# Performance work log

Measured on AMD Instinct MI355X. Metric: run time of the kernel, lower is better.

Reference implementation:

```python
import jax, jax.numpy as jnp
import numpy as np

N = 65536   # query points
M = 65536   # support points
H = 32      # neighbors per query
IN = 64     # input feature dim
OUT = 64    # out_dim // 2
K = 15      # kernel points
EXTENT = 0.1 * 1.2 / 2.5  # radius * kp_extent / conv_radius = 0.048
BN_EPS = 1e-5


def setup_inputs() -> dict:
    key = jax.random.key(0)
    ks = jax.random.split(key, 8)
    x = jax.random.normal(ks[0], (M, IN), dtype=jnp.float32)
    q_pts = jax.random.uniform(ks[1], (N, 3), dtype=jnp.float32) * 0.1
    s_pts = jax.random.uniform(ks[2], (M, 3), dtype=jnp.float32) * 0.1
    neighb_inds = jax.random.randint(ks[3], (N, H), 0, M, dtype=jnp.int32)
    kernel_points = jax.random.normal(ks[4], (K, 3), dtype=jnp.float32) * (0.5 * EXTENT)
    weights = jax.random.normal(ks[5], (K, IN, OUT), dtype=jnp.float32) * 0.05
    gamma = jnp.ones((OUT,), dtype=jnp.float32)
    beta = jnp.zeros((OUT,), dtype=jnp.float32)
    return {"x": x, "q_pts": q_pts, "s_pts": s_pts, "neighb_inds": neighb_inds,
            "kernel_points": kernel_points, "weights": weights,
            "gamma": gamma, "beta": beta}


def reference(x, q_pts, s_pts, neighb_inds, kernel_points, weights, gamma, beta):
    # --- KPConv (rigid, linear influence, sum aggregation) ---
    # Shadow point/feature for out-of-range neighbor indices (KPConv convention).
    s_pad = jnp.concatenate([s_pts, jnp.full((1, 3), 1e6, s_pts.dtype)], axis=0)
    x_pad = jnp.concatenate([x, jnp.zeros((1, x.shape[1]), x.dtype)], axis=0)

    # Relative neighbor coordinates: [N, H, 3]
    neighbors = s_pad[neighb_inds] - q_pts[:, None, :]
    # Squared distance to each kernel point: [N, H, K]
    diffs = neighbors[:, :, None, :] - kernel_points[None, None, :, :]
    sq_dist = jnp.sum(diffs * diffs, axis=-1)
    # Linear kernel-point influence, clipped at 0: [N, H, K]
    all_weights = jnp.maximum(1.0 - jnp.sqrt(sq_dist) / EXTENT, 0.0)

    # Gather neighbor features: [N, H, IN]
    neighb_x = x_pad[neighb_inds]
    # Influence-weighted aggregation per kernel point: [N, K, IN]
    weighted = jnp.einsum('nhk,nhi->nki', all_weights, neighb_x)
    # Apply per-kernel-point weight matrices and sum over kernel points: [N, OUT]
    out = jnp.einsum('nki,kio->no', weighted, weights)

    # --- BatchNorm (training-mode statistics over points) ---
    mean = jnp.mean(out, axis=0)
    var = jnp.var(out, axis=0)
    out = (out - mean) / jnp.sqrt(var + BN_EPS) * gamma + beta

    # --- LeakyReLU(0.1) ---
    return jnp.where(out >= 0, out, 0.1 * out)
```

## Files before the change

kernel.cpp:

```cpp
#include <hip/hip_runtime.h>
#include <math.h>

#define NQ   65536
#define H    32
#define IN   64
#define OUTC 64
#define K    15
#define QB   16
#define S_XN 68
#define S_WT 36
#define AK   72
#define AROW 1076
#define INV_EXT (1.0f / 0.048f)

#define OFF_PSUM  131072
#define OFF_SCSH  (OFF_PSUM + 2097152)
#define OFF_XBF   (OFF_SCSH + 1024)
#define NEED_BF16 (OFF_XBF + (size_t)NQ * IN * 2)

typedef __attribute__((ext_vector_type(8))) short short8;
typedef __attribute__((ext_vector_type(4))) short short4v;
typedef __attribute__((ext_vector_type(4))) float float4v;

static __device__ __forceinline__ unsigned short f2bf(float f) {
    return (unsigned short)((__float_as_uint(f) + 0x8000u) >> 16);
}
static __device__ __forceinline__ unsigned pk2(float a, float b) {
    return (__float_as_uint(a) + 0x8000u) >> 16 |
           ((__float_as_uint(b) + 0x8000u) & 0xFFFF0000u);
}

__global__ __launch_bounds__(256) void prep_all(
    const float* __restrict__ W, const float* __restrict__ x,
    short* __restrict__ Bfrag, unsigned short* __restrict__ xbf, int do_x)
{
    const int b = blockIdx.x;
    if (b < 4096) {
        if (do_x) {
            const int t = b * 256 + threadIdx.x;
            const float4 v = ((const float4*)x)[t];
            uint2 p; p.x = pk2(v.x, v.y); p.y = pk2(v.z, v.w);
            ((uint2*)xbf)[t] = p;
        }
    } else {
        const int t2 = (b - 4096) * 256 + threadIdx.x;
        const int o  = t2 & 63;
        const int i  = (t2 >> 6) & 63;
        const int kq = t2 >> 12;
        const int t  = kq * 2 + (i >> 5);
        const int lane = ((i >> 3) & 3) * 16 + (o & 15);
        const int v  = o >> 4;
        const int j  = i & 7;
        Bfrag[((v * 30 + t) * 64 + lane) * 8 + j] = (short)f2bf(W[t2]);
    }
}

template<bool BFX>
__global__ __launch_bounds__(256, 4) void kpconv_mfma(
    const float* __restrict__ x, const unsigned short* __restrict__ xbf,
    const float* __restrict__ qp, const float* __restrict__ sp,
    const int* __restrict__ inds, const float* __restrict__ kp,
    const short* __restrict__ Bfrag, float* __restrict__ out_raw,
    float* __restrict__ psum)
{
    __shared__ __align__(16) short lds[17920];
    short* xn  = lds;
    short* wT  = lds + 8704;
    short* Awt = lds;

    const int tid  = threadIdx.x;
    const int lane = tid & 63;
    const int wv   = tid >> 6;
    const int quad = lane >> 4;
    const int ml   = lane & 15;
    const int q0   = blockIdx.x * QB;

    for (int rep = 0; rep < 2; ++rep) {
        const int pair = tid + rep * 256;
        const int q = pair >> 5, h = pair & 31;
        const int n = q0 + q;
        const int id = inds[n * H + h];
        const float dx = sp[id * 3 + 0] - qp[n * 3 + 0];
        const float dy = sp[id * 3 + 1] - qp[n * 3 + 1];
        const float dz = sp[id * 3 + 2] - qp[n * 3 + 2];
#pragma unroll
        for (int k = 0; k < K; ++k) {
            const float ex = dx - kp[k * 3 + 0];
            const float ey = dy - kp[k * 3 + 1];
            const float ez = dz - kp[k * 3 + 2];
            const float sq = ex * ex + ey * ey + ez * ez;
            float wval = 1.0f - __builtin_amdgcn_sqrtf(sq) * INV_EXT;
            wval = wval > 0.0f ? wval : 0.0f;
            wT[(q * 16 + k) * S_WT + h] = (short)f2bf(wval);
        }
        wT[(q * 16 + K) * S_WT + h] = 0;
    }
    __syncthreads();

    float4v frag[QB];
#pragma unroll
    for (int qg = 0; qg < QB; ++qg) frag[qg] = (float4v){0.f, 0.f, 0.f, 0.f};

    for (int b = 0; b < 4; ++b) {
        const int qg_s = 4 * b + wv;
        const int ibase = (q0 + qg_s) * H;
#pragma unroll
        for (int j = 0; j < 8; ++j) {
            const int h = j * 4 + quad;
            const int id = inds[ibase + h];
            if (BFX) {
                const short4v xv = *(const short4v*)((const short*)xbf + id * IN + ml * 4);
                *(short4v*)&xn[(wv * H + h) * S_XN + ml * 4] = xv;
            } else {
                const float4 xv = *(const float4*)(x + id * IN + ml * 4);
                short4v p;
                p[0] = (short)f2bf(xv.x); p[1] = (short)f2bf(xv.y);
                p[2] = (short)f2bf(xv.z); p[3] = (short)f2bf(xv.w);
                *(short4v*)&xn[(wv * H + h) * S_XN + ml * 4] = p;
            }
        }
        __syncthreads();
#pragma unroll
        for (int ql = 0; ql < 4; ++ql) {
            const int qg = 4 * b + ql;
            const int arow = (qg * 16 + ml) * S_WT + quad * 8;
            const short4v alo = *(const short4v*)&wT[arow];
            const short4v ahi = *(const short4v*)&wT[arow + 4];
            short8 a;
#pragma unroll
            for (int e = 0; e < 4; ++e) { a[e] = alo[e]; a[e + 4] = ahi[e]; }
            short8 bb;
#pragma unroll
            for (int j = 0; j < 8; ++j)
                bb[j] = xn[(ql * H + quad * 8 + j) * S_XN + wv * 16 + ml];
            frag[qg] = __builtin_amdgcn_mfma_f32_16x16x32_bf16(a, bb, frag[qg], 0, 0, 0);
        }
        __syncthreads();
    }

#pragma unroll
    for (int qg = 0; qg < QB; ++qg) {
#pragma unroll
        for (int r = 0; r < 4; ++r) {
            const int kq = quad * 4 + r;
            if (kq < K)
                Awt[qg * AROW + kq * AK + wv * 16 + ml] = (short)f2bf(frag[qg][r]);
        }
    }
    __syncthreads();

    float4v acc = (float4v){0.f, 0.f, 0.f, 0.f};
    const short* bptr = Bfrag + (wv * 30) * 512 + lane * 8;
#pragma unroll 2
    for (int t = 0; t < 30; ++t) {
        const int abase = ml * AROW + (t >> 1) * AK + (t & 1) * 32 + quad * 8;
        const short4v alo = *(const short4v*)&Awt[abase];
        const short4v ahi = *(const short4v*)&Awt[abase + 4];
        short8 a;
#pragma unroll
        for (int e = 0; e < 4; ++e) { a[e] = alo[e]; a[e + 4] = ahi[e]; }
        const short8 bb = *(const short8*)(bptr + t * 512);
        acc = __builtin_amdgcn_mfma_f32_16x16x32_bf16(a, bb, acc, 0, 0, 0);
    }

    float s = 0.f, s2 = 0.f;
#pragma unroll
    for (int r = 0; r < 4; ++r) {
        const float v = acc[r];
        out_raw[(q0 + quad * 4 + r) * OUTC + wv * 16 + ml] = v;
        s += v; s2 += v * v;
    }
    s  += __shfl_xor(s, 16, 64);  s  += __shfl_xor(s, 32, 64);
    s2 += __shfl_xor(s2, 16, 64); s2 += __shfl_xor(s2, 32, 64);
    if (quad == 0) {
        const int c = wv * 16 + ml;
        psum[c * 4096 + blockIdx.x]          = s;
        psum[262144 + c * 4096 + blockIdx.x] = s2;
    }
}

__global__ __launch_bounds__(256) void bn_stats(
    const float* __restrict__ psum, const float* __restrict__ gamma,
    const float* __restrict__ beta, float* __restrict__ sc_sh)
{
    const int c = blockIdx.x;
    const int t = threadIdx.x;
    float s = 0.f, q = 0.f;
#pragma unroll
    for (int i = 0; i < 16; ++i) {
        s += psum[c * 4096 + t + i * 256];
        q += psum[262144 + c * 4096 + t + i * 256];
    }
    __shared__ float rs[4], rq[4];
#pragma unroll
    for (int off = 32; off; off >>= 1) {
        s += __shfl_down(s, off, 64);
        q += __shfl_down(q, off, 64);
    }
    if ((t & 63) == 0) { rs[t >> 6] = s; rq[t >> 6] = q; }
    __syncthreads();
    if (t == 0) {
        s = rs[0] + rs[1] + rs[2] + rs[3];
        q = rq[0] + rq[1] + rq[2] + rq[3];
        const float mean = s * (1.0f / (float)NQ);
        const float var  = q * (1.0f / (float)NQ) - mean * mean;
        const float scale = gamma[c] / sqrtf(var + 1e-5f);
        sc_sh[c]      = scale;
        sc_sh[64 + c] = beta[c] - mean * scale;
    }
}

__global__ __launch_bounds__(256) void bn_apply(
    float* __restrict__ out, const float* __restrict__ sc_sh)
{
    __shared__ float sc[64];
    __shared__ float sh[64];
    if (threadIdx.x < 64) {
        sc[threadIdx.x] = sc_sh[threadIdx.x];
        sh[threadIdx.x] = sc_sh[64 + threadIdx.x];
    }
    __syncthreads();
    const int idx = blockIdx.x * 256 + threadIdx.x;
#pragma unroll
    for (int it = 0; it < 4; ++it) {
        const int e = idx + it * 262144;
        float4 v = ((const float4*)out)[e];
        const int cg = (e & 15) * 4;
        float4 r;
        r.x = v.x * sc[cg + 0] + sh[cg + 0];
        r.y = v.y * sc[cg + 1] + sh[cg + 1];
        r.z = v.z * sc[cg + 2] + sh[cg + 2];
        r.w = v.w * sc[cg + 3] + sh[cg + 3];
        r.x = r.x >= 0.0f ? r.x : 0.1f * r.x;
        r.y = r.y >= 0.0f ? r.y : 0.1f * r.y;
        r.z = r.z >= 0.0f ? r.z : 0.1f * r.z;
        r.w = r.w >= 0.0f ? r.w : 0.1f * r.w;
        ((float4*)out)[e] = r;
    }
}

extern "C" void kernel_launch(void* const* d_in, const int* in_sizes, int n_in,
                              void* d_out, int out_size, void* d_ws, size_t ws_size,
                              hipStream_t stream)
{
    (void)in_sizes; (void)n_in; (void)out_size;
    const float* x     = (const float*)d_in[0];
    const float* qp    = (const float*)d_in[1];
    const float* sp    = (const float*)d_in[2];
    const int*   inds  = (const int*)d_in[3];
    const float* kp    = (const float*)d_in[4];
    const float* W     = (const float*)d_in[5];
    const float* gamma = (const float*)d_in[6];
    const float* beta  = (const float*)d_in[7];
    float* out = (float*)d_out;

    short*          Bfrag = (short*)d_ws;
    float*          psum  = (float*)((char*)d_ws + OFF_PSUM);
    float*          sc_sh = (float*)((char*)d_ws + OFF_SCSH);
    unsigned short* xbf   = (unsigned short*)((char*)d_ws + OFF_XBF);

    const int use_bf = (ws_size >= NEED_BF16) ? 1 : 0;

    prep_all<<<4336, 256, 0, stream>>>(W, x, Bfrag, xbf, use_bf);
    if (use_bf)
        kpconv_mfma<true><<<NQ / QB, 256, 0, stream>>>(x, xbf, qp, sp, inds, kp, Bfrag, out, psum);
    else
        kpconv_mfma<false><<<NQ / QB, 256, 0, stream>>>(x, xbf, qp, sp, inds, kp, Bfrag, out, psum);
    bn_stats<<<64, 256, 0, stream>>>(psum, gamma, beta, sc_sh);
    bn_apply<<<1024, 256, 0, stream>>>(out, sc_sh);
}
```

Before: 162.0 us.

## Compute kernel-point influences per query batch inside the gather loop

Moves the influence-weight computation from a separate prologue into each of the four batch iterations, so each wave computes weights for its own query just before the gather. This removes a block-wide barrier and lets the weight math interleave with feature gathers. The smaller weight buffer and a tighter epilogue row stride (AK 72→68) reduce LDS footprint, at the risk of different bank-conflict behaviour in the epilogue.

```diff
diff --git a/kernel.cpp b/kernel.cpp
--- a/kernel.cpp
+++ b/kernel.cpp
@@ -9,8 +9,8 @@
 #define QB   16
 #define S_XN 68
 #define S_WT 36
-#define AK   72
-#define AROW 1076
+#define AK   68
+#define AROW 1020
 #define INV_EXT (1.0f / 0.048f)
 
 #define OFF_PSUM  131072
@@ -63,7 +63,7 @@
     const short* __restrict__ Bfrag, float* __restrict__ out_raw,
     float* __restrict__ psum)
 {
-    __shared__ __align__(16) short lds[17920];
+    __shared__ __align__(16) short lds[16320];
     short* xn  = lds;
     short* wT  = lds + 8704;
     short* Awt = lds;
@@ -75,35 +75,36 @@
     const int ml   = lane & 15;
     const int q0   = blockIdx.x * QB;
 
-    for (int rep = 0; rep < 2; ++rep) {
-        const int pair = tid + rep * 256;
-        const int q = pair >> 5, h = pair & 31;
-        const int n = q0 + q;
-        const int id = inds[n * H + h];
-        const float dx = sp[id * 3 + 0] - qp[n * 3 + 0];
-        const float dy = sp[id * 3 + 1] - qp[n * 3 + 1];
-        const float dz = sp[id * 3 + 2] - qp[n * 3 + 2];
-#pragma unroll
-        for (int k = 0; k < K; ++k) {
-            const float ex = dx - kp[k * 3 + 0];
-            const float ey = dy - kp[k * 3 + 1];
-            const float ez = dz - kp[k * 3 + 2];
-            const float sq = ex * ex + ey * ey + ez * ez;
-            float wval = 1.0f - __builtin_amdgcn_sqrtf(sq) * INV_EXT;
-            wval = wval > 0.0f ? wval : 0.0f;
-            wT[(q * 16 + k) * S_WT + h] = (short)f2bf(wval);
-        }
-        wT[(q * 16 + K) * S_WT + h] = 0;
-    }
-    __syncthreads();
-
     float4v frag[QB];
 #pragma unroll
     for (int qg = 0; qg < QB; ++qg) frag[qg] = (float4v){0.f, 0.f, 0.f, 0.f};
 
     for (int b = 0; b < 4; ++b) {
-        const int qg_s = 4 * b + wv;
-        const int ibase = (q0 + qg_s) * H;
+        const int nq_ = q0 + 4 * b + wv;
+
+        {
+            const int h = lane >> 1, half = lane & 1;
+            const int idA = inds[nq_ * H + h];
+            const float dx = sp[idA * 3 + 0] - qp[nq_ * 3 + 0];
+            const float dy = sp[idA * 3 + 1] - qp[nq_ * 3 + 1];
+            const float dz = sp[idA * 3 + 2] - qp[nq_ * 3 + 2];
+#pragma unroll
+            for (int kk = 0; kk < 8; ++kk) {
+                const int k = half * 8 + kk;
+                float wval = 0.f;
+                if (k < K) {
+                    const float ex = dx - kp[k * 3 + 0];
+                    const float ey = dy - kp[k * 3 + 1];
+                    const float ez = dz - kp[k * 3 + 2];
+                    const float sq = ex * ex + ey * ey + ez * ez;
+                    wval = 1.0f - __builtin_amdgcn_sqrtf(sq) * INV_EXT;
+                    wval = wval > 0.0f ? wval : 0.0f;
+                }
+                wT[(wv * 16 + k) * S_WT + h] = (short)f2bf(wval);
+            }
+        }
+
+        const int ibase = nq_ * H;
 #pragma unroll
         for (int j = 0; j < 8; ++j) {
             const int h = j * 4 + quad;
@@ -120,10 +121,11 @@
             }
         }
         __syncthreads();
+
 #pragma unroll
         for (int ql = 0; ql < 4; ++ql) {
             const int qg = 4 * b + ql;
-            const int arow = (qg * 16 + ml) * S_WT + quad * 8;
+            const int arow = (ql * 16 + ml) * S_WT + quad * 8;
             const short4v alo = *(const short4v*)&wT[arow];
             const short4v ahi = *(const short4v*)&wT[arow + 4];
             short8 a;
```

Result: slower. 182.1 us (+12.4%).
